# Performance work log

Hardware: AMD Instinct MI355X
Metric: run time of the kernel (lower is better)

The kernel has to match this reference:

```python
import jax, jax.numpy as jnp
import numpy as np

B, S, D, H = 8, 1024, 1024, 16
DH = D // H  # head dim = 64 (extend_head=False split)
EPS = 1e-5


def setup_inputs() -> dict:
    key = jax.random.key(0)
    ks = jax.random.split(key, 9)
    s = 0.02
    return {
        "query": jax.random.normal(ks[0], (B, S, D), jnp.float32),
        "key":   jax.random.normal(ks[1], (B, S, D), jnp.float32),
        "value": jax.random.normal(ks[2], (B, S, D), jnp.float32),
        "mask":  jnp.ones((B, S), jnp.bool_),
        # Linear weights stored [in, out] (torch uses [out, in]; math identical)
        "Wq": jax.random.normal(ks[3], (D, D), jnp.float32) * s,
        "bq": jnp.zeros((D,), jnp.float32),
        "Wk": jax.random.normal(ks[4], (D, D), jnp.float32) * s,
        "bk": jnp.zeros((D,), jnp.float32),
        "Wv": jax.random.normal(ks[5], (D, D), jnp.float32) * s,
        "bv": jnp.zeros((D,), jnp.float32),
        # BatchNorm1d affine params
        "gamma": jnp.ones((D,), jnp.float32),
        "beta":  jnp.zeros((D,), jnp.float32),
    }


def _split_heads(x):
    # torch: cat(x.split(DH, -1), 0) -> head-major stacking [H*B, S, DH]
    return x.reshape(B, S, H, DH).transpose(2, 0, 1, 3)  # [H,B,S,DH]


def reference(query, key, value, mask, Wq, bq, Wk, bk, Wv, bv, gamma, beta):
    q = query @ Wq + bq   # [B,S,D]
    k = key   @ Wk + bk
    v = value @ Wv + bv

    qh = _split_heads(q)  # [H,B,S,DH]
    kh = _split_heads(k)
    vh = _split_heads(v)

    # NOTE: source builds an additive mask but never applies it to the
    # scores -> faithful reference uses UNMASKED softmax.
    scores = jnp.einsum('hbqd,hbkd->hbqk', qh, kh) / np.sqrt(DH).astype(np.float32)
    weights = jax.nn.softmax(scores, axis=-1)          # [H,B,S,S]
    out = jnp.einsum('hbqk,hbkd->hbqd', weights, vh)   # [H,B,S,DH]

    # cat(split(out, B, 0), -1): re-concatenate heads on feature dim
    out = out.transpose(1, 2, 0, 3).reshape(B, S, D)

    # row-gather by boolean mask (all-ones -> static shape [B*S, D])
    out = out.reshape(-1, D)[mask.reshape(-1)]

    # BatchNorm1d (training-mode batch stats, biased var) + SiLU
    mean = out.mean(axis=0)
    var = jnp.mean(jnp.square(out - mean), axis=0)
    out = (out - mean) / jnp.sqrt(var + EPS) * gamma + beta
    return jax.nn.silu(out)
```

## Files before the change

### kernel.cpp

```cpp
#include <hip/hip_runtime.h>
#include <hip/hip_bf16.h>
#include <cstdint>
#include <cstddef>

#define B_ 8
#define S_ 1024
#define D_ 1024
#define H_ 16
#define DH_ 64

using f32x4   = __attribute__((ext_vector_type(4))) float;
using f32x16  = __attribute__((ext_vector_type(16))) float;
using float4v = __attribute__((ext_vector_type(4))) float;
using bf16x8  = __attribute__((ext_vector_type(8))) short;
using ushort8 = __attribute__((ext_vector_type(8))) unsigned short;
using uint2v  = __attribute__((ext_vector_type(2))) unsigned int;

__device__ __forceinline__ unsigned short f2bf(float f) {
    union { float f; unsigned u; } v; v.f = f;
    unsigned r = v.u + 0x7FFF + ((v.u >> 16) & 1);
    return (unsigned short)(r >> 16);
}
__device__ __forceinline__ float bf2f(unsigned short b) {
    union { unsigned u; float f; } v; v.u = ((unsigned)b) << 16;
    return v.f;
}

#if __has_builtin(__builtin_amdgcn_exp2f)
__device__ __forceinline__ float fexp2(float x) { return __builtin_amdgcn_exp2f(x); }
#else
__device__ __forceinline__ float fexp2(float x) { return __expf(x * 0.69314718056f); }
#endif

__device__ __forceinline__ unsigned cvtpk_bf16(float lo, float hi) {
    unsigned r;
    asm("v_cvt_pk_bf16_f32 %0, %1, %2" : "=v"(r) : "v"(lo), "v"(hi));
    return r;
}

__device__ __forceinline__ void gl_lds16(const unsigned short* g, unsigned short* l) {
    __builtin_amdgcn_global_load_lds(
        (const __attribute__((address_space(1))) unsigned int*)g,
        (__attribute__((address_space(3))) unsigned int*)l,
        16, 0, 0);
}

__global__ __launch_bounds__(256) void prep_kernel(
    const float* __restrict__ Wq, const float* __restrict__ Wk, const float* __restrict__ Wv,
    const float* __restrict__ Xq, const float* __restrict__ Xk, const float* __restrict__ Xv,
    unsigned short* __restrict__ Wt,
    unsigned short* __restrict__ Bq, unsigned short* __restrict__ Bk, unsigned short* __restrict__ Bv,
    float* __restrict__ gsum)
{
    __shared__ float tile[32][33];
    int bid = blockIdx.x;
    int t = threadIdx.x;

    if (bid == 0) {
#pragma unroll
        for (int j = 0; j < 8; ++j) gsum[t + 256 * j] = 0.f;
    }

    if (bid < 3072) {
        int z = bid >> 10, rc = bid & 1023;
        const float* W = (z == 0) ? Wq : (z == 1) ? Wk : Wv;
        unsigned short* Y = Wt + (size_t)z * 1048576;
        int tx = t & 31, ty = t >> 5;
        int r0 = (rc >> 5) * 32, c0 = (rc & 31) * 32;
#pragma unroll
        for (int j = 0; j < 4; ++j) {
            int r = ty + j * 8;
            tile[r][tx] = W[(size_t)(r0 + r) * D_ + c0 + tx];
        }
        __syncthreads();
#pragma unroll
        for (int j = 0; j < 4; ++j) {
            int r = ty + j * 8;
            Y[(size_t)(c0 + r) * D_ + r0 + tx] = f2bf(tile[tx][r]);
        }
    } else {
        int cid = bid - 3072;
        int which = cid >> 12;
        int blk = cid & 4095;
        const float* X = (which == 0) ? Xq : (which == 1) ? Xk : Xv;
        unsigned short* Y = (which == 0) ? Bq : (which == 1) ? Bk : Bv;
        size_t idx = ((size_t)blk * 256 + t) * 8;
        float4v v0 = *reinterpret_cast<const float4v*>(X + idx);
        float4v v1 = *reinterpret_cast<const float4v*>(X + idx + 4);
        ushort8 o;
#pragma unroll
        for (int j = 0; j < 4; ++j) { o[j] = f2bf(v0[j]); o[j + 4] = f2bf(v1[j]); }
        *reinterpret_cast<ushort8*>(Y + idx) = o;
    }
}

__global__ __launch_bounds__(512, 2) void qkv_gemm8(
    const unsigned short* __restrict__ Xbq, const unsigned short* __restrict__ Xbk, const unsigned short* __restrict__ Xbv,
    const unsigned short* __restrict__ Wts,
    const float* __restrict__ bq, const float* __restrict__ bk, const float* __restrict__ bv,
    unsigned short* __restrict__ Qh, unsigned short* __restrict__ Kf, unsigned short* __restrict__ Vf)
{
    extern __shared__ unsigned short smem[];
    unsigned short* lA = smem;
    unsigned short* lB = smem + 32768;

    int bid = blockIdx.x;
    int L = (bid & 7) * 96 + (bid >> 3);
    int mode = L >> 8;
    int rem = L & 255;
    int bm = rem >> 3;
    int bn = rem & 7;

    const unsigned short* Xb = (mode == 0) ? Xbq : (mode == 1) ? Xbk : Xbv;
    const unsigned short* Wt = Wts + (size_t)mode * 1048576;
    const float* bias = (mode == 0) ? bq : (mode == 1) ? bk : bv;

    int t = threadIdx.x;
    int m0 = bm * 256, n0 = bn * 128;
    int wid = t >> 6, lane = t & 63;
    int wr = wid >> 2, wc = wid & 3;
    int lr = lane & 15, lg = lane >> 4;

    int srow = t >> 3;
    int scol = (((t & 7) ^ (srow & 7))) * 8;
    const unsigned short* Asrc = Xb + (size_t)(m0 + srow) * D_ + scol;
    const unsigned short* Bsrc = Wt + (size_t)(n0 + srow) * D_ + scol;
    unsigned short* lAdst = lA + t * 8;
    unsigned short* lBdst = lB + t * 8;

#define STAGE_A(buf, pass, kt) gl_lds16(Asrc + (size_t)(pass) * 64 * D_ + (kt) * 64, lAdst + (buf) * 16384 + (pass) * 4096)
#define STAGE_B(buf, pass, kt) gl_lds16(Bsrc + (size_t)(pass) * 64 * D_ + (kt) * 64, lBdst + (buf) * 8192 + (pass) * 4096)

#define READ_A(dst, base, half)                                                      \
    _Pragma("unroll") for (int m_ = 0; m_ < 4; ++m_) {                               \
        int R_ = wr * 128 + (half) * 64 + m_ * 16 + lr;                              \
        _Pragma("unroll") for (int ks_ = 0; ks_ < 2; ++ks_) {                        \
            int pc_ = ((ks_ * 4 + lg) ^ (R_ & 7)) * 8;                               \
            dst[m_][ks_] = *reinterpret_cast<const bf16x8*>((base) + R_ * 64 + pc_); \
        }                                                                            \
    }
#define READ_B(base)                                                                 \
    _Pragma("unroll") for (int n_ = 0; n_ < 2; ++n_) {                               \
        int R_ = wc * 32 + n_ * 16 + lr;                                             \
        _Pragma("unroll") for (int ks_ = 0; ks_ < 2; ++ks_) {                        \
            int pc_ = ((ks_ * 4 + lg) ^ (R_ & 7)) * 8;                               \
            b[n_][ks_] = *reinterpret_cast<const bf16x8*>((base) + R_ * 64 + pc_);   \
        }                                                                            \
    }
#define MFMA_BLK(A_, MB)                                                             \
    _Pragma("unroll") for (int m_ = 0; m_ < 4; ++m_)                                 \
        _Pragma("unroll") for (int n_ = 0; n_ < 2; ++n_)                             \
            _Pragma("unroll") for (int ks_ = 0; ks_ < 2; ++ks_)                      \
                acc[(MB) + m_][n_] = __builtin_amdgcn_mfma_f32_16x16x32_bf16(        \
                    A_[m_][ks_], b[n_][ks_], acc[(MB) + m_][n_], 0, 0, 0);

#define BAR1() do { __builtin_amdgcn_s_barrier();                                    \
                    asm volatile("s_waitcnt lgkmcnt(0)" ::: "memory");               \
                    __builtin_amdgcn_sched_barrier(0);                               \
                    __builtin_amdgcn_s_setprio(1); } while (0)
#define BAR2() do { __builtin_amdgcn_s_setprio(0);                                   \
                    __builtin_amdgcn_s_barrier();                                    \
                    __builtin_amdgcn_sched_barrier(0); } while (0)

    f32x4 acc[8][2] = {};
    bf16x8 a[4][2], a2[4][2], b[2][2];

    STAGE_A(0, 0, 0); STAGE_A(0, 1, 0); STAGE_A(0, 2, 0); STAGE_A(0, 3, 0);
    STAGE_B(0, 0, 0); STAGE_B(0, 1, 0);
    STAGE_A(1, 0, 1); STAGE_A(1, 1, 1); STAGE_A(1, 2, 1);
    asm volatile("s_waitcnt vmcnt(3)" ::: "memory");
    __builtin_amdgcn_s_barrier();
    __builtin_amdgcn_sched_barrier(0);

#pragma unroll 1
    for (int i = 0; i < 8; ++i) {
        int c1 = 2 * i + 1, nt0 = 2 * i + 2, nt1 = 2 * i + 3;
        bool g0 = (nt0 < 16), g1 = (nt1 < 16);
        const unsigned short* A0p = lA;
        const unsigned short* B0p = lB;
        const unsigned short* A1p = lA + 16384;
        const unsigned short* B1p = lB + 8192;

        READ_A(a, A0p, 0); READ_B(B0p);
        STAGE_A(1, 3, c1); STAGE_B(1, 0, c1); STAGE_B(1, 1, c1);
        BAR1(); MFMA_BLK(a, 0); BAR2();

        READ_A(a2, A0p, 1);
        BAR1(); MFMA_BLK(a2, 4);
        __builtin_amdgcn_s_setprio(0);
        if (g0) {
            STAGE_A(0, 0, nt0); STAGE_A(0, 1, nt0); STAGE_A(0, 2, nt0);
            asm volatile("s_waitcnt vmcnt(3)" ::: "memory");
        } else {
            asm volatile("s_waitcnt vmcnt(0)" ::: "memory");
        }
        __builtin_amdgcn_s_barrier();
        __builtin_amdgcn_sched_barrier(0);

        READ_A(a, A1p, 0); READ_B(B1p);
        if (g0) { STAGE_A(0, 3, nt0); STAGE_B(0, 0, nt0); STAGE_B(0, 1, nt0); }
        BAR1(); MFMA_BLK(a, 0); BAR2();

        READ_A(a2, A1p, 1);
        BAR1(); MFMA_BLK(a2, 4);
        __builtin_amdgcn_s_setprio(0);
        if (g1) {
            STAGE_A(1, 0, nt1); STAGE_A(1, 1, nt1); STAGE_A(1, 2, nt1);
            asm volatile("s_waitcnt vmcnt(3)" ::: "memory");
        } else {
            asm volatile("s_waitcnt vmcnt(0)" ::: "memory");
        }
        __builtin_amdgcn_s_barrier();
        __builtin_amdgcn_sched_barrier(0);
    }
#undef BAR1
#undef BAR2
#undef MFMA_BLK
#undef READ_A
#undef READ_B
#undef STAGE_A
#undef STAGE_B

#pragma unroll
    for (int am = 0; am < 8; ++am) {
#pragma unroll
        for (int an = 0; an < 2; ++an) {
            int col = n0 + wc * 32 + an * 16 + lr;
            int h = col >> 6, d = col & 63;
            float bval = bias[col];
#pragma unroll
            for (int r = 0; r < 4; ++r) {
                int row = m0 + wr * 128 + am * 16 + lg * 4 + r;
                int bb = row >> 10, s = row & 1023;
                int inst = h * B_ + bb;
                float v = acc[am][an][r] + bval;
                if (mode == 0) {
                    Qh[((size_t)inst * S_ + s) * DH_ + d] = f2bf(v * 0.18033688f);
                } else if (mode == 1) {
                    int kt2 = s >> 6, n_ = (s >> 5) & 1, cl = s & 31;
                    int dk = d >> 4, hi2 = (d >> 3) & 1, j = d & 7;
                    size_t off = ((((size_t)inst * 16 + kt2) * 2 + n_) * 4 + dk) * 512
                               + (size_t)(hi2 * 32 + cl) * 8 + j;
                    Kf[off] = f2bf(v);
                } else {
                    int kt2 = s >> 6, ks2 = (s >> 4) & 3, hi2 = (s >> 3) & 1, j = s & 7;
                    int nd = d >> 5, cl = d & 31;
                    size_t off = ((((size_t)inst * 16 + kt2) * 2 + nd) * 4 + ks2) * 512
                               + (size_t)(hi2 * 32 + cl) * 8 + j;
                    Vf[off] = f2bf(v);
                }
            }
        }
    }
}

__global__ __launch_bounds__(512, 2) void attn_kernel(
    const unsigned short* __restrict__ Qh,
    const unsigned short* __restrict__ Kf,
    const unsigned short* __restrict__ Vf,
    unsigned short* __restrict__ O,
    float* __restrict__ gsum, float* __restrict__ gsq)
{
    __shared__ unsigned short ldsK[2][4096];
    __shared__ unsigned short ldsV[2][4096];
    __shared__ float part[8][64][4];

    int inst = blockIdx.x;
    int h = inst >> 3, bb = inst & 7;
    int t = threadIdx.x, wid = t >> 6, lane = t & 63;
    int cl = lane & 31, hi = lane >> 5;
    int q0 = (blockIdx.y * 8 + wid) * 32;

    const unsigned short* Qb = Qh + (size_t)inst * S_ * DH_ + (size_t)(q0 + cl) * DH_ + hi * 8;
    const unsigned short* Kt = Kf + (size_t)inst * 65536;
    const unsigned short* Vt = Vf + (size_t)inst * 65536;

    bf16x8 qf[4];
#pragma unroll
    for (int dk = 0; dk < 4; ++dk)
        qf[dk] = *reinterpret_cast<const bf16x8*>(Qb + dk * 16);

#define STAGE_KV(buf, kt) do {                                              \
        gl_lds16(Kt + (size_t)(kt) * 4096 + t * 8, &ldsK[buf][t * 8]);      \
        gl_lds16(Vt + (size_t)(kt) * 4096 + t * 8, &ldsV[buf][t * 8]);      \
    } while (0)

    STAGE_KV(0, 0);
    STAGE_KV(1, 1);

    f32x16 o0 = {}, o1 = {};
    float li = 0.f;

#pragma unroll 1
    for (int kt = 0; kt < S_ / 64; ++kt) {
        int buf = kt & 1;
        asm volatile("s_waitcnt vmcnt(2)" ::: "memory");
        __builtin_amdgcn_s_barrier();
        __builtin_amdgcn_sched_barrier(0);

        const unsigned short* kb = &ldsK[buf][0] + lane * 8;
        const unsigned short* vp = &ldsV[buf][0] + lane * 8;

        bf16x8 ka[2][4];
#pragma unroll
        for (int n = 0; n < 2; ++n)
#pragma unroll
            for (int dk = 0; dk < 4; ++dk)
                ka[n][dk] = *reinterpret_cast<const bf16x8*>(kb + (n * 4 + dk) * 512);

        bf16x8 vb0[4], vb1[4];
#pragma unroll
        for (int ks = 0; ks < 4; ++ks) {
            vb0[ks] = *reinterpret_cast<const bf16x8*>(vp + ks * 512);
            vb1[ks] = *reinterpret_cast<const bf16x8*>(vp + (4 + ks) * 512);
        }

        f32x16 s0 = {}, s1 = {};
        __builtin_amdgcn_s_setprio(1);
#pragma unroll
        for (int dk = 0; dk < 4; ++dk)
            s0 = __builtin_amdgcn_mfma_f32_32x32x16_bf16(ka[0][dk], qf[dk], s0, 0, 0, 0);
#pragma unroll
        for (int dk = 0; dk < 4; ++dk)
            s1 = __builtin_amdgcn_mfma_f32_32x32x16_bf16(ka[1][dk], qf[dk], s1, 0, 0, 0);
        __builtin_amdgcn_s_setprio(0);

        float p0[16], p1[16];
#pragma unroll
        for (int i = 0; i < 16; ++i) { p0[i] = fexp2(s0[i]); p1[i] = fexp2(s1[i]); }
        float ts[16];
#pragma unroll
        for (int i = 0; i < 16; ++i) ts[i] = p0[i] + p1[i];
#pragma unroll
        for (int st = 8; st > 0; st >>= 1)
#pragma unroll
            for (int i = 0; i < st; ++i) ts[i] += ts[i + st];
        li += ts[0] + __shfl_xor(ts[0], 32, 64);

        unsigned w[16];
#pragma unroll
        for (int i = 0; i < 8; ++i) w[i]     = cvtpk_bf16(p0[2 * i], p0[2 * i + 1]);
#pragma unroll
        for (int i = 0; i < 8; ++i) w[8 + i] = cvtpk_bf16(p1[2 * i], p1[2 * i + 1]);

        bf16x8 pa[4];
#pragma unroll
        for (int g = 0; g < 4; ++g) {
            uint2v ra = __builtin_amdgcn_permlane32_swap(w[4 * g + 0], w[4 * g + 2], false, false);
            uint2v rb = __builtin_amdgcn_permlane32_swap(w[4 * g + 1], w[4 * g + 3], false, false);
            union { unsigned u[4]; bf16x8 v; } cv;
            cv.u[0] = ra[0]; cv.u[1] = rb[0]; cv.u[2] = ra[1]; cv.u[3] = rb[1];
            pa[g] = cv.v;
        }

        __builtin_amdgcn_s_setprio(1);
#pragma unroll
        for (int g = 0; g < 4; ++g) {
            o0 = __builtin_amdgcn_mfma_f32_32x32x16_bf16(pa[g], vb0[g], o0, 0, 0, 0);
            o1 = __builtin_amdgcn_mfma_f32_32x32x16_bf16(pa[g], vb1[g], o1, 0, 0, 0);
        }
        __builtin_amdgcn_s_setprio(0);

        asm volatile("s_waitcnt lgkmcnt(0)" ::: "memory");
        __builtin_amdgcn_s_barrier();
        __builtin_amdgcn_sched_barrier(0);
        if (kt + 2 < S_ / 64) STAGE_KV(buf, kt + 2);
    }
#undef STAGE_KV

    float rli = 1.0f / li;
    float sa = 0.f, qa = 0.f, sb = 0.f, qb2 = 0.f;
#pragma unroll
    for (int r = 0; r < 16; ++r) {
        int qr = (r & 3) + 8 * (r >> 2) + 4 * hi;
        float inv = __shfl(rli, qr, 64);
        int s = q0 + qr;
        size_t base = ((size_t)bb * S_ + s) * D_ + h * DH_;
        float y0 = o0[r] * inv, y1 = o1[r] * inv;
        O[base + cl]      = f2bf(y0);
        O[base + 32 + cl] = f2bf(y1);
        sa += y0; qa += y0 * y0; sb += y1; qb2 += y1 * y1;
    }
    part[wid][lane][0] = sa; part[wid][lane][1] = qa;
    part[wid][lane][2] = sb; part[wid][lane][3] = qb2;
    __syncthreads();
    if (t < 128) {
        int cl2 = t >> 2, st = t & 3;
        float acc = 0.f;
#pragma unroll
        for (int w2 = 0; w2 < 8; ++w2)
            acc += part[w2][cl2][st] + part[w2][cl2 + 32][st];
        int col = h * 64 + cl2 + ((st >= 2) ? 32 : 0);
        float* tgt = (st & 1) ? gsq : gsum;
        atomicAdd(&tgt[col], acc);
    }
}

__global__ __launch_bounds__(256) void bn_apply(const unsigned short* __restrict__ O,
                                                const float* __restrict__ gsum,
                                                const float* __restrict__ gsq,
                                                const float* __restrict__ gamma,
                                                const float* __restrict__ beta,
                                                float* __restrict__ out) {
    const float invN = 1.f / 8192.f;
    size_t idx = ((size_t)blockIdx.x * 256 + threadIdx.x) * 8;
    int col0 = (int)(idx & 1023);
    ushort8 v = *reinterpret_cast<const ushort8*>(O + idx);
#pragma unroll
    for (int j = 0; j < 8; ++j) {
        int c = col0 + j;
        float mean = gsum[c] * invN;
        float var = gsq[c] * invN - mean * mean;
        float rstd = rsqrtf(var + 1e-5f);
        float x = bf2f(v[j]);
        float y = (x - mean) * rstd * gamma[c] + beta[c];
        out[idx + j] = y / (1.f + __expf(-y));
    }
}

extern "C" void kernel_launch(void* const* d_in, const int* in_sizes, int n_in,
                              void* d_out, int out_size, void* d_ws, size_t ws_size,
                              hipStream_t stream) {
    const float* query = (const float*)d_in[0];
    const float* key   = (const float*)d_in[1];
    const float* value = (const float*)d_in[2];
    const float* Wq = (const float*)d_in[4];
    const float* bq = (const float*)d_in[5];
    const float* Wk = (const float*)d_in[6];
    const float* bk = (const float*)d_in[7];
    const float* Wv = (const float*)d_in[8];
    const float* bv = (const float*)d_in[9];
    const float* gamma = (const float*)d_in[10];
    const float* beta  = (const float*)d_in[11];

    char* w = (char*)d_ws;
    unsigned short* Wt  = (unsigned short*)w;
    unsigned short* Qh  = (unsigned short*)(w + (6u << 20));
    unsigned short* Kf  = Qh + 8388608;
    unsigned short* Vf  = Kf + 8388608;
    unsigned short* Xbq = Vf + 8388608;
    unsigned short* Xbk = Xbq + 8388608;
    unsigned short* Xbv = Xbk + 8388608;
    unsigned short* O   = Xbq;
    float* gsum = (float*)(Xbv + 8388608);
    float* gsq  = gsum + 1024;

    prep_kernel<<<dim3(15360), 256, 0, stream>>>(Wq, Wk, Wv, query, key, value,
                                                 Wt, Xbq, Xbk, Xbv, gsum);

    hipFuncSetAttribute(reinterpret_cast<const void*>(&qkv_gemm8),
                        hipFuncAttributeMaxDynamicSharedMemorySize, 98304);
    qkv_gemm8<<<dim3(768), 512, 98304, stream>>>(Xbq, Xbk, Xbv, Wt,
                                                 bq, bk, bv, Qh, Kf, Vf);

    attn_kernel<<<dim3(128, 4), 512, 0, stream>>>(Qh, Kf, Vf, O, gsum, gsq);

    bn_apply<<<4096, 256, 0, stream>>>(O, gsum, gsq, gamma, beta, (float*)d_out);
}
```

Before: 155.3 us.

## Shrink QKV GEMM tile to 128x128 with 4 waves and double grid

Changes the QKV projection GEMM from 256x128 tiles with 8 waves (512 threads) to 128x128 tiles with 4 waves (256 threads), doubling the grid to 1536 blocks and cutting LDS to 64KB. Each wave now computes a 64x64 subtile, split into two 64x32 halves over B rather than two A halves. The goal is more blocks per CU and finer load balancing across CUs. The cost is less operand reuse per tile, since each loaded B row feeds half as many A rows, which raises global and LDS traffic.

```diff
diff --git a/kernel.cpp b/kernel.cpp
--- a/kernel.cpp
+++ b/kernel.cpp
@@ -94,7 +94,7 @@
     }
 }
 
-__global__ __launch_bounds__(512, 2) void qkv_gemm8(
+__global__ __launch_bounds__(256, 2) void qkv_gemm8(
     const unsigned short* __restrict__ Xbq, const unsigned short* __restrict__ Xbk, const unsigned short* __restrict__ Xbv,
     const unsigned short* __restrict__ Wts,
     const float* __restrict__ bq, const float* __restrict__ bk, const float* __restrict__ bv,
@@ -102,12 +102,12 @@
 {
     extern __shared__ unsigned short smem[];
     unsigned short* lA = smem;
-    unsigned short* lB = smem + 32768;
+    unsigned short* lB = smem + 16384;
 
     int bid = blockIdx.x;
-    int L = (bid & 7) * 96 + (bid >> 3);
-    int mode = L >> 8;
-    int rem = L & 255;
+    int L = (bid & 7) * 192 + (bid >> 3);
+    int mode = L >> 9;
+    int rem = L & 511;
     int bm = rem >> 3;
     int bn = rem & 7;
 
@@ -116,9 +116,9 @@
     const float* bias = (mode == 0) ? bq : (mode == 1) ? bk : bv;
 
     int t = threadIdx.x;
-    int m0 = bm * 256, n0 = bn * 128;
+    int m0 = bm * 128, n0 = bn * 128;
     int wid = t >> 6, lane = t & 63;
-    int wr = wid >> 2, wc = wid & 3;
+    int wr = wid >> 1, wc = wid & 1;
     int lr = lane & 15, lg = lane >> 4;
 
     int srow = t >> 3;
@@ -128,31 +128,33 @@
     unsigned short* lAdst = lA + t * 8;
     unsigned short* lBdst = lB + t * 8;
 
-#define STAGE_A(buf, pass, kt) gl_lds16(Asrc + (size_t)(pass) * 64 * D_ + (kt) * 64, lAdst + (buf) * 16384 + (pass) * 4096)
-#define STAGE_B(buf, pass, kt) gl_lds16(Bsrc + (size_t)(pass) * 64 * D_ + (kt) * 64, lBdst + (buf) * 8192 + (pass) * 4096)
-
-#define READ_A(dst, base, half)                                                      \
+#define STAGE_A(buf, p, kt) gl_lds16(Asrc + (size_t)(p) * 32 * D_ + (kt) * 64, lAdst + (buf) * 8192 + (p) * 2048)
+#define STAGE_B(buf, p, kt) gl_lds16(Bsrc + (size_t)(p) * 32 * D_ + (kt) * 64, lBdst + (buf) * 8192 + (p) * 2048)
+#define STAGE_A4(buf, kt) do { STAGE_A(buf,0,kt); STAGE_A(buf,1,kt); STAGE_A(buf,2,kt); STAGE_A(buf,3,kt); } while (0)
+#define STAGE_B4(buf, kt) do { STAGE_B(buf,0,kt); STAGE_B(buf,1,kt); STAGE_B(buf,2,kt); STAGE_B(buf,3,kt); } while (0)
+
+#define READ_A(base)                                                                 \
     _Pragma("unroll") for (int m_ = 0; m_ < 4; ++m_) {                               \
-        int R_ = wr * 128 + (half) * 64 + m_ * 16 + lr;                              \
+        int R_ = wr * 64 + m_ * 16 + lr;                                             \
         _Pragma("unroll") for (int ks_ = 0; ks_ < 2; ++ks_) {                        \
             int pc_ = ((ks_ * 4 + lg) ^ (R_ & 7)) * 8;                               \
-            dst[m_][ks_] = *reinterpret_cast<const bf16x8*>((base) + R_ * 64 + pc_); \
+            a[m_][ks_] = *reinterpret_cast<const bf16x8*>((base) + R_ * 64 + pc_);   \
         }                                                                            \
     }
-#define READ_B(base)                                                                 \
+#define READ_B2(base, nb)                                                            \
     _Pragma("unroll") for (int n_ = 0; n_ < 2; ++n_) {                               \
-        int R_ = wc * 32 + n_ * 16 + lr;                                             \
+        int R_ = wc * 64 + ((nb) + n_) * 16 + lr;                                    \
         _Pragma("unroll") for (int ks_ = 0; ks_ < 2; ++ks_) {                        \
             int pc_ = ((ks_ * 4 + lg) ^ (R_ & 7)) * 8;                               \
             b[n_][ks_] = *reinterpret_cast<const bf16x8*>((base) + R_ * 64 + pc_);   \
         }                                                                            \
     }
-#define MFMA_BLK(A_, MB)                                                             \
+#define MFMA_BLK(NB)                                                                 \
     _Pragma("unroll") for (int m_ = 0; m_ < 4; ++m_)                                 \
         _Pragma("unroll") for (int n_ = 0; n_ < 2; ++n_)                             \
             _Pragma("unroll") for (int ks_ = 0; ks_ < 2; ++ks_)                      \
-                acc[(MB) + m_][n_] = __builtin_amdgcn_mfma_f32_16x16x32_bf16(        \
-                    A_[m_][ks_], b[n_][ks_], acc[(MB) + m_][n_], 0, 0, 0);
+                acc[m_][(NB) + n_] = __builtin_amdgcn_mfma_f32_16x16x32_bf16(        \
+                    a[m_][ks_], b[n_][ks_], acc[m_][(NB) + n_], 0, 0, 0);
 
 #define BAR1() do { __builtin_amdgcn_s_barrier();                                    \
                     asm volatile("s_waitcnt lgkmcnt(0)" ::: "memory");               \
@@ -162,51 +164,50 @@
                     __builtin_amdgcn_s_barrier();                                    \
                     __builtin_amdgcn_sched_barrier(0); } while (0)
 
-    f32x4 acc[8][2] = {};
-    bf16x8 a[4][2], a2[4][2], b[2][2];
-
-    STAGE_A(0, 0, 0); STAGE_A(0, 1, 0); STAGE_A(0, 2, 0); STAGE_A(0, 3, 0);
-    STAGE_B(0, 0, 0); STAGE_B(0, 1, 0);
-    STAGE_A(1, 0, 1); STAGE_A(1, 1, 1); STAGE_A(1, 2, 1);
-    asm volatile("s_waitcnt vmcnt(3)" ::: "memory");
+    f32x4 acc[4][4] = {};
+    bf16x8 a[4][2], b[2][2];
+
+    STAGE_A4(0, 0); STAGE_B4(0, 0);
+    STAGE_A4(1, 1);
+    asm volatile("s_waitcnt vmcnt(4)" ::: "memory");
     __builtin_amdgcn_s_barrier();
     __builtin_amdgcn_sched_barrier(0);
 
 #pragma unroll 1
     for (int i = 0; i < 8; ++i) {
         int c1 = 2 * i + 1, nt0 = 2 * i + 2, nt1 = 2 * i + 3;
-        bool g0 = (nt0 < 16), g1 = (nt1 < 16);
+        bool g = (i < 7);
         const unsigned short* A0p = lA;
         const unsigned short* B0p = lB;
-        const unsigned short* A1p = lA + 16384;
+        const unsigned short* A1p = lA + 8192;
         const unsigned short* B1p = lB + 8192;
 
-        READ_A(a, A0p, 0); READ_B(B0p);
-        STAGE_A(1, 3, c1); STAGE_B(1, 0, c1); STAGE_B(1, 1, c1);
-        BAR1(); MFMA_BLK(a, 0); BAR2();
-
-        READ_A(a2, A0p, 1);
-        BAR1(); MFMA_BLK(a2, 4);
+        READ_A(A0p); READ_B2(B0p, 0);
+        STAGE_B4(1, c1);
+        BAR1(); MFMA_BLK(0); BAR2();
+
+        READ_B2(B0p, 2);
+        BAR1(); MFMA_BLK(2);
         __builtin_amdgcn_s_setprio(0);
-        if (g0) {
-            STAGE_A(0, 0, nt0); STAGE_A(0, 1, nt0); STAGE_A(0, 2, nt0);
-            asm volatile("s_waitcnt vmcnt(3)" ::: "memory");
+        if (g) {
+            STAGE_A4(0, nt0);
+            asm volatile("s_waitcnt vmcnt(4)" ::: "memory");
         } else {
             asm volatile("s_waitcnt vmcnt(0)" ::: "memory");
         }
         __builtin_amdgcn_s_barrier();
         __builtin_amdgcn_sched_barrier(0);
 
-        READ_A(a, A1p, 0); READ_B(B1p);
-        if (g0) { STAGE_A(0, 3, nt0); STAGE_B(0, 0, nt0); STAGE_B(0, 1, nt0); }
-        BAR1(); MFMA_BLK(a, 0); BAR2();
-
-        READ_A(a2, A1p, 1);
-        BAR1(); MFMA_BLK(a2, 4);
+        READ_A(A1p); READ_B2(B1p, 0);
+        if (g) STAGE_B4(0, nt0);
+        BAR1(); MFMA_BLK(0); BAR2();
+
+        READ_B2(B1p, 2);
+        BAR1(); MFMA_BLK(2);
         __builtin_amdgcn_s_setprio(0);
-        if (g1) {
-            STAGE_A(1, 0, nt1); STAGE_A(1, 1, nt1); STAGE_A(1, 2, nt1);
-            asm volatile("s_waitcnt vmcnt(3)" ::: "memory");
+        if (g) {
+            STAGE_A4(1, nt1);
+            asm volatile("s_waitcnt vmcnt(4)" ::: "memory");
         } else {
             asm volatile("s_waitcnt vmcnt(0)" ::: "memory");
         }
@@ -217,20 +218,22 @@
 #undef BAR2
 #undef MFMA_BLK
 #undef READ_A
-#undef READ_B
+#undef READ_B2
 #undef STAGE_A
 #undef STAGE_B
-
-#pragma unroll
-    for (int am = 0; am < 8; ++am) {
-#pragma unroll
-        for (int an = 0; an < 2; ++an) {
-            int col = n0 + wc * 32 + an * 16 + lr;
+#undef STAGE_A4
+#undef STAGE_B4
+
+#pragma unroll
+    for (int am = 0; am < 4; ++am) {
+#pragma unroll
+        for (int an = 0; an < 4; ++an) {
+            int col = n0 + wc * 64 + an * 16 + lr;
             int h = col >> 6, d = col & 63;
             float bval = bias[col];
 #pragma unroll
             for (int r = 0; r < 4; ++r) {
-                int row = m0 + wr * 128 + am * 16 + lg * 4 + r;
+                int row = m0 + wr * 64 + am * 16 + lg * 4 + r;
                 int bb = row >> 10, s = row & 1023;
                 int inst = h * B_ + bb;
                 float v = acc[am][an][r] + bval;
@@ -449,9 +452,9 @@
                                                  Wt, Xbq, Xbk, Xbv, gsum);
 
     hipFuncSetAttribute(reinterpret_cast<const void*>(&qkv_gemm8),
-                        hipFuncAttributeMaxDynamicSharedMemorySize, 98304);
-    qkv_gemm8<<<dim3(768), 512, 98304, stream>>>(Xbq, Xbk, Xbv, Wt,
-                                                 bq, bk, bv, Qh, Kf, Vf);
+                        hipFuncAttributeMaxDynamicSharedMemorySize, 65536);
+    qkv_gemm8<<<dim3(1536), 256, 65536, stream>>>(Xbq, Xbk, Xbv, Wt,
+                                                  bq, bk, bv, Qh, Kf, Vf);
 
     attn_kernel<<<dim3(128, 4), 512, 0, stream>>>(Qh, Kf, Vf, O, gsum, gsq);
 
```

Measured after the change: 148.0 us. -4.7%, faster.

## Fuse fp32-to-bf16 activation conversion into QKV GEMM via fp32 LDS staging

Applied to the files above, without the earlier changes.

The separate prep pass that converted query/key/value from fp32 to bf16 is removed. The GEMM now streams fp32 activation tiles directly into LDS and converts them to bf16 with v_cvt_pk_bf16_f32 while reading fragments for MFMA. This saves writing and re-reading about 48 MB of bf16 intermediates. In exchange, LDS use rises to 160 KB, occupancy drops to one block per CU, A-tile global traffic inside the GEMM doubles, and conversion work is repeated across the 8 N-tiles that share each A tile.

```diff
diff --git a/kernel.cpp b/kernel.cpp
--- a/kernel.cpp
+++ b/kernel.cpp
@@ -44,13 +44,16 @@
         (__attribute__((address_space(3))) unsigned int*)l,
         16, 0, 0);
 }
+__device__ __forceinline__ void gl_lds16f(const float* g, float* l) {
+    __builtin_amdgcn_global_load_lds(
+        (const __attribute__((address_space(1))) unsigned int*)g,
+        (__attribute__((address_space(3))) unsigned int*)l,
+        16, 0, 0);
+}
 
 __global__ __launch_bounds__(256) void prep_kernel(
     const float* __restrict__ Wq, const float* __restrict__ Wk, const float* __restrict__ Wv,
-    const float* __restrict__ Xq, const float* __restrict__ Xk, const float* __restrict__ Xv,
-    unsigned short* __restrict__ Wt,
-    unsigned short* __restrict__ Bq, unsigned short* __restrict__ Bk, unsigned short* __restrict__ Bv,
-    float* __restrict__ gsum)
+    unsigned short* __restrict__ Wt, float* __restrict__ gsum)
 {
     __shared__ float tile[32][33];
     int bid = blockIdx.x;
@@ -61,48 +64,33 @@
         for (int j = 0; j < 8; ++j) gsum[t + 256 * j] = 0.f;
     }
 
-    if (bid < 3072) {
-        int z = bid >> 10, rc = bid & 1023;
-        const float* W = (z == 0) ? Wq : (z == 1) ? Wk : Wv;
-        unsigned short* Y = Wt + (size_t)z * 1048576;
-        int tx = t & 31, ty = t >> 5;
-        int r0 = (rc >> 5) * 32, c0 = (rc & 31) * 32;
-#pragma unroll
-        for (int j = 0; j < 4; ++j) {
-            int r = ty + j * 8;
-            tile[r][tx] = W[(size_t)(r0 + r) * D_ + c0 + tx];
-        }
-        __syncthreads();
-#pragma unroll
-        for (int j = 0; j < 4; ++j) {
-            int r = ty + j * 8;
-            Y[(size_t)(c0 + r) * D_ + r0 + tx] = f2bf(tile[tx][r]);
-        }
-    } else {
-        int cid = bid - 3072;
-        int which = cid >> 12;
-        int blk = cid & 4095;
-        const float* X = (which == 0) ? Xq : (which == 1) ? Xk : Xv;
-        unsigned short* Y = (which == 0) ? Bq : (which == 1) ? Bk : Bv;
-        size_t idx = ((size_t)blk * 256 + t) * 8;
-        float4v v0 = *reinterpret_cast<const float4v*>(X + idx);
-        float4v v1 = *reinterpret_cast<const float4v*>(X + idx + 4);
-        ushort8 o;
-#pragma unroll
-        for (int j = 0; j < 4; ++j) { o[j] = f2bf(v0[j]); o[j + 4] = f2bf(v1[j]); }
-        *reinterpret_cast<ushort8*>(Y + idx) = o;
-    }
-}
-
-__global__ __launch_bounds__(512, 2) void qkv_gemm8(
-    const unsigned short* __restrict__ Xbq, const unsigned short* __restrict__ Xbk, const unsigned short* __restrict__ Xbv,
+    int z = bid >> 10, rc = bid & 1023;
+    const float* W = (z == 0) ? Wq : (z == 1) ? Wk : Wv;
+    unsigned short* Y = Wt + (size_t)z * 1048576;
+    int tx = t & 31, ty = t >> 5;
+    int r0 = (rc >> 5) * 32, c0 = (rc & 31) * 32;
+#pragma unroll
+    for (int j = 0; j < 4; ++j) {
+        int r = ty + j * 8;
+        tile[r][tx] = W[(size_t)(r0 + r) * D_ + c0 + tx];
+    }
+    __syncthreads();
+#pragma unroll
+    for (int j = 0; j < 4; ++j) {
+        int r = ty + j * 8;
+        Y[(size_t)(c0 + r) * D_ + r0 + tx] = f2bf(tile[tx][r]);
+    }
+}
+
+__global__ __launch_bounds__(512, 1) void qkv_gemm8(
+    const float* __restrict__ Xq, const float* __restrict__ Xk, const float* __restrict__ Xv,
     const unsigned short* __restrict__ Wts,
     const float* __restrict__ bq, const float* __restrict__ bk, const float* __restrict__ bv,
     unsigned short* __restrict__ Qh, unsigned short* __restrict__ Kf, unsigned short* __restrict__ Vf)
 {
     extern __shared__ unsigned short smem[];
-    unsigned short* lA = smem;
-    unsigned short* lB = smem + 32768;
+    float* lAf = (float*)smem;
+    unsigned short* lB = smem + 65536;
 
     int bid = blockIdx.x;
     int L = (bid & 7) * 96 + (bid >> 3);
@@ -111,7 +99,7 @@
     int bm = rem >> 3;
     int bn = rem & 7;
 
-    const unsigned short* Xb = (mode == 0) ? Xbq : (mode == 1) ? Xbk : Xbv;
+    const float* X = (mode == 0) ? Xq : (mode == 1) ? Xk : Xv;
     const unsigned short* Wt = Wts + (size_t)mode * 1048576;
     const float* bias = (mode == 0) ? bq : (mode == 1) ? bk : bv;
 
@@ -121,30 +109,44 @@
     int wr = wid >> 2, wc = wid & 3;
     int lr = lane & 15, lg = lane >> 4;
 
-    int srow = t >> 3;
-    int scol = (((t & 7) ^ (srow & 7))) * 8;
-    const unsigned short* Asrc = Xb + (size_t)(m0 + srow) * D_ + scol;
-    const unsigned short* Bsrc = Wt + (size_t)(n0 + srow) * D_ + scol;
-    unsigned short* lAdst = lA + t * 8;
+    int atrow = t >> 4;
+    int aagr = (t & 15) ^ (atrow & 7);
+    const float* Asrcf = X + (size_t)(m0 + atrow) * D_ + aagr * 4;
+    float* lAdst = lAf + t * 4;
+
+    int bsrow = t >> 3;
+    int bscol = ((t & 7) ^ (bsrow & 7)) * 8;
+    const unsigned short* Bsrc = Wt + (size_t)(n0 + bsrow) * D_ + bscol;
     unsigned short* lBdst = lB + t * 8;
 
-#define STAGE_A(buf, pass, kt) gl_lds16(Asrc + (size_t)(pass) * 64 * D_ + (kt) * 64, lAdst + (buf) * 16384 + (pass) * 4096)
-#define STAGE_B(buf, pass, kt) gl_lds16(Bsrc + (size_t)(pass) * 64 * D_ + (kt) * 64, lBdst + (buf) * 8192 + (pass) * 4096)
-
-#define READ_A(dst, base, half)                                                      \
+#define STAGE_A(buf, p, kt) gl_lds16f(Asrcf + (size_t)(p) * 32 * D_ + (kt) * 64, lAdst + (buf) * 16384 + (p) * 2048)
+#define STAGE_B(buf, p, kt) gl_lds16(Bsrc + (size_t)(p) * 64 * D_ + (kt) * 64, lBdst + (buf) * 8192 + (p) * 4096)
+#define STAGE_A04(buf, kt) do { STAGE_A(buf,0,kt); STAGE_A(buf,1,kt); STAGE_A(buf,2,kt); STAGE_A(buf,3,kt); STAGE_A(buf,4,kt); } while (0)
+#define STAGE_TAIL(buf, kt) do { STAGE_A(buf,5,kt); STAGE_A(buf,6,kt); STAGE_A(buf,7,kt); STAGE_B(buf,0,kt); STAGE_B(buf,1,kt); } while (0)
+
+#define READ_A(dst, bufsel, half)                                                    \
     _Pragma("unroll") for (int m_ = 0; m_ < 4; ++m_) {                               \
         int R_ = wr * 128 + (half) * 64 + m_ * 16 + lr;                              \
+        int rx_ = R_ & 7;                                                            \
         _Pragma("unroll") for (int ks_ = 0; ks_ < 2; ++ks_) {                        \
-            int pc_ = ((ks_ * 4 + lg) ^ (R_ & 7)) * 8;                               \
-            dst[m_][ks_] = *reinterpret_cast<const bf16x8*>((base) + R_ * 64 + pc_); \
+            int pe_ = (ks_ * 8 + lg * 2) ^ rx_;                                      \
+            const float* pA_ = lAf + (bufsel) * 16384 + R_ * 64;                     \
+            f32x4 ra_ = *reinterpret_cast<const f32x4*>(pA_ + pe_ * 4);              \
+            f32x4 rb_ = *reinterpret_cast<const f32x4*>(pA_ + (pe_ ^ 1) * 4);        \
+            union { unsigned u[4]; bf16x8 v; } cv_;                                  \
+            cv_.u[0] = cvtpk_bf16(ra_[0], ra_[1]);                                   \
+            cv_.u[1] = cvtpk_bf16(ra_[2], ra_[3]);                                   \
+            cv_.u[2] = cvtpk_bf16(rb_[0], rb_[1]);                                   \
+            cv_.u[3] = cvtpk_bf16(rb_[2], rb_[3]);                                   \
+            dst[m_][ks_] = cv_.v;                                                    \
         }                                                                            \
     }
-#define READ_B(base)                                                                 \
+#define READ_B(bufsel)                                                               \
     _Pragma("unroll") for (int n_ = 0; n_ < 2; ++n_) {                               \
         int R_ = wc * 32 + n_ * 16 + lr;                                             \
         _Pragma("unroll") for (int ks_ = 0; ks_ < 2; ++ks_) {                        \
             int pc_ = ((ks_ * 4 + lg) ^ (R_ & 7)) * 8;                               \
-            b[n_][ks_] = *reinterpret_cast<const bf16x8*>((base) + R_ * 64 + pc_);   \
+            b[n_][ks_] = *reinterpret_cast<const bf16x8*>(lB + (bufsel) * 8192 + R_ * 64 + pc_); \
         }                                                                            \
     }
 #define MFMA_BLK(A_, MB)                                                             \
@@ -165,48 +167,43 @@
     f32x4 acc[8][2] = {};
     bf16x8 a[4][2], a2[4][2], b[2][2];
 
-    STAGE_A(0, 0, 0); STAGE_A(0, 1, 0); STAGE_A(0, 2, 0); STAGE_A(0, 3, 0);
-    STAGE_B(0, 0, 0); STAGE_B(0, 1, 0);
-    STAGE_A(1, 0, 1); STAGE_A(1, 1, 1); STAGE_A(1, 2, 1);
-    asm volatile("s_waitcnt vmcnt(3)" ::: "memory");
+    STAGE_A04(0, 0); STAGE_TAIL(0, 0);
+    STAGE_A04(1, 1);
+    asm volatile("s_waitcnt vmcnt(5)" ::: "memory");
     __builtin_amdgcn_s_barrier();
     __builtin_amdgcn_sched_barrier(0);
 
 #pragma unroll 1
     for (int i = 0; i < 8; ++i) {
         int c1 = 2 * i + 1, nt0 = 2 * i + 2, nt1 = 2 * i + 3;
-        bool g0 = (nt0 < 16), g1 = (nt1 < 16);
-        const unsigned short* A0p = lA;
-        const unsigned short* B0p = lB;
-        const unsigned short* A1p = lA + 16384;
-        const unsigned short* B1p = lB + 8192;
-
-        READ_A(a, A0p, 0); READ_B(B0p);
-        STAGE_A(1, 3, c1); STAGE_B(1, 0, c1); STAGE_B(1, 1, c1);
+        bool g = (i < 7);
+
+        READ_A(a, 0, 0); READ_B(0);
+        STAGE_TAIL(1, c1);
         BAR1(); MFMA_BLK(a, 0); BAR2();
 
-        READ_A(a2, A0p, 1);
+        READ_A(a2, 0, 1);
         BAR1(); MFMA_BLK(a2, 4);
         __builtin_amdgcn_s_setprio(0);
-        if (g0) {
-            STAGE_A(0, 0, nt0); STAGE_A(0, 1, nt0); STAGE_A(0, 2, nt0);
-            asm volatile("s_waitcnt vmcnt(3)" ::: "memory");
+        if (g) {
+            STAGE_A04(0, nt0);
+            asm volatile("s_waitcnt vmcnt(5)" ::: "memory");
         } else {
             asm volatile("s_waitcnt vmcnt(0)" ::: "memory");
         }
         __builtin_amdgcn_s_barrier();
         __builtin_amdgcn_sched_barrier(0);
 
-        READ_A(a, A1p, 0); READ_B(B1p);
-        if (g0) { STAGE_A(0, 3, nt0); STAGE_B(0, 0, nt0); STAGE_B(0, 1, nt0); }
+        READ_A(a, 1, 0); READ_B(1);
+        if (g) STAGE_TAIL(0, nt0);
         BAR1(); MFMA_BLK(a, 0); BAR2();
 
-        READ_A(a2, A1p, 1);
+        READ_A(a2, 1, 1);
         BAR1(); MFMA_BLK(a2, 4);
         __builtin_amdgcn_s_setprio(0);
-        if (g1) {
-            STAGE_A(1, 0, nt1); STAGE_A(1, 1, nt1); STAGE_A(1, 2, nt1);
-            asm volatile("s_waitcnt vmcnt(3)" ::: "memory");
+        if (g) {
+            STAGE_A04(1, nt1);
+            asm volatile("s_waitcnt vmcnt(5)" ::: "memory");
         } else {
             asm volatile("s_waitcnt vmcnt(0)" ::: "memory");
         }
@@ -220,6 +217,8 @@
 #undef READ_B
 #undef STAGE_A
 #undef STAGE_B
+#undef STAGE_A04
+#undef STAGE_TAIL
 
 #pragma unroll
     for (int am = 0; am < 8; ++am) {
@@ -438,20 +437,16 @@
     unsigned short* Qh  = (unsigned short*)(w + (6u << 20));
     unsigned short* Kf  = Qh + 8388608;
     unsigned short* Vf  = Kf + 8388608;
-    unsigned short* Xbq = Vf + 8388608;
-    unsigned short* Xbk = Xbq + 8388608;
-    unsigned short* Xbv = Xbk + 8388608;
-    unsigned short* O   = Xbq;
-    float* gsum = (float*)(Xbv + 8388608);
+    unsigned short* O   = Vf + 8388608;
+    float* gsum = (float*)(O + 8388608);
     float* gsq  = gsum + 1024;
 
-    prep_kernel<<<dim3(15360), 256, 0, stream>>>(Wq, Wk, Wv, query, key, value,
-                                                 Wt, Xbq, Xbk, Xbv, gsum);
+    prep_kernel<<<dim3(3072), 256, 0, stream>>>(Wq, Wk, Wv, Wt, gsum);
 
     hipFuncSetAttribute(reinterpret_cast<const void*>(&qkv_gemm8),
-                        hipFuncAttributeMaxDynamicSharedMemorySize, 98304);
-    qkv_gemm8<<<dim3(768), 512, 98304, stream>>>(Xbq, Xbk, Xbv, Wt,
-                                                 bq, bk, bv, Qh, Kf, Vf);
+                        hipFuncAttributeMaxDynamicSharedMemorySize, 163840);
+    qkv_gemm8<<<dim3(768), 512, 163840, stream>>>(query, key, value, Wt,
+                                                  bq, bk, bv, Qh, Kf, Vf);
 
     attn_kernel<<<dim3(128, 4), 512, 0, stream>>>(Qh, Kf, Vf, O, gsum, gsq);
 
```

After: 175.5 us. 1.13x slower.
